# Kernel optimization log

Measured on AMD Instinct MI355X. Metric: run time of the kernel, lower is better.

Reference implementation:

```python
import jax, jax.numpy as jnp
import numpy as np

# Dimensions (Gemma-2B-like, uniform q-head rank)
B, S, HID = 2, 2048, 2048
H, HKV, D = 16, 8, 128
RQ, RK, RV = 64, 64, 64
G = H // HKV  # heads per kv group
SCALE = D ** -0.5
NEG_INF = -1e9


def setup_inputs() -> dict:
    key = jax.random.key(0)
    ks = jax.random.split(key, 9)
    hidden_states = jax.random.normal(ks[0], (B, S, HID), dtype=jnp.float32)
    W_A_q = jax.random.normal(ks[1], (H * RQ, HID), dtype=jnp.float32) * 0.02
    W_A_k = jax.random.normal(ks[2], (HKV * RK, HID), dtype=jnp.float32) * 0.02
    W_A_v = jax.random.normal(ks[3], (HKV * RV, HID), dtype=jnp.float32) * 0.02
    B_q = jax.random.normal(ks[4], (H, RQ, D), dtype=jnp.float32)
    B_k = jax.random.normal(ks[5], (HKV, RK, D), dtype=jnp.float32)
    B_v = jax.random.normal(ks[6], (HKV, RV, D), dtype=jnp.float32)
    W_o = jax.random.normal(ks[7], (HID, H * D), dtype=jnp.float32) * 0.02
    # RoPE tables (cos/sin form of gemma's complex freqs_cis)
    inv_freq = 1.0 / (10000.0 ** (jnp.arange(0, D, 2, dtype=jnp.float32) / D))
    freqs = jnp.arange(S, dtype=jnp.float32)[:, None] * inv_freq[None, :]  # [S, D/2]
    freqs_cos = jnp.cos(freqs)
    freqs_sin = jnp.sin(freqs)
    # Causal additive mask [1, 1, S, S]
    causal = jnp.tril(jnp.ones((S, S), dtype=bool))
    mask = jnp.where(causal, 0.0, NEG_INF).astype(jnp.float32)[None, None]
    kv_write_indices = jnp.arange(S, dtype=jnp.int32)
    return {
        'hidden_states': hidden_states, 'W_A_q': W_A_q, 'W_A_k': W_A_k,
        'W_A_v': W_A_v, 'B_q': B_q, 'B_k': B_k, 'B_v': B_v, 'W_o': W_o,
        'freqs_cos': freqs_cos, 'freqs_sin': freqs_sin, 'mask': mask,
        'kv_write_indices': kv_write_indices,
    }


def _rope(x, cos, sin):
    # x: [b, s, h, d]; gemma pairs first half with second half of head_dim
    x1, x2 = jnp.split(x, 2, axis=-1)
    c = cos[None, :, None, :]
    s = sin[None, :, None, :]
    return jnp.concatenate([x1 * c - x2 * s, x1 * s + x2 * c], axis=-1)


def reference(hidden_states, W_A_q, W_A_k, W_A_v, B_q, B_k, B_v, W_o,
              freqs_cos, freqs_sin, mask, kv_write_indices):
    b, s, _ = hidden_states.shape
    # Low-rank A factors
    A_q = jnp.einsum('bsd,rd->bsr', hidden_states, W_A_q).reshape(b, s, H, RQ)
    A_k = jnp.einsum('bsd,rd->bsr', hidden_states, W_A_k).reshape(b, s, HKV, RK)
    A_v = jnp.einsum('bsd,rd->bsr', hidden_states, W_A_v).reshape(b, s, HKV, RV)
    # Factorized KV cache: scatter A factors at write indices (prefill)
    cache_kA = jnp.zeros((b, s, HKV, RK), hidden_states.dtype).at[:, kv_write_indices].set(A_k)
    cache_vA = jnp.zeros((b, s, HKV, RV), hidden_states.dtype).at[:, kv_write_indices].set(A_v)
    # GQA expansion of cached A factors
    gidx = jnp.repeat(jnp.arange(HKV), G)  # [H]
    A_k_rep = cache_kA[:, :, gidx]  # [b, kv, H, RK]
    A_v_rep = cache_vA[:, :, gidx]
    # Reconstruct Q/K/V from constant B factors (per-head loop vectorized:
    # all q ranks equal, so einsum over heads is the same math)
    q = jnp.einsum('bshr,hrd->bshd', A_q, B_q) / RQ
    k = jnp.einsum('bkhr,hrd->bkhd', A_k_rep, B_k[gidx]) / RK
    v = jnp.einsum('bkhr,hrd->bkhd', A_v_rep, B_v[gidx]) / RV
    # RoPE post-reconstruction
    q = _rope(q, freqs_cos, freqs_sin)
    k = _rope(k, freqs_cos, freqs_sin)
    # Attention
    scores = jnp.einsum('bqhd,bkhd->bhqk', q, k) * SCALE + mask
    probs = jax.nn.softmax(scores, axis=-1)
    out = jnp.einsum('bhqk,bkhd->bqhd', probs, v).reshape(b, s, H * D)
    return jnp.einsum('bse,he->bsh', out, W_o)
```

## Files before the change

kernel.cpp:

```cpp
#include <hip/hip_runtime.h>
#include <hip/hip_bf16.h>

typedef __attribute__((ext_vector_type(8))) short bf16x8;
typedef __attribute__((ext_vector_type(4))) float f32x4;

#define MFMA_16x16x32(a,b,c) __builtin_amdgcn_mfma_f32_16x16x32_bf16((a),(b),(c),0,0,0)

__device__ __forceinline__ unsigned short f2b(float f){
  unsigned int u = __builtin_bit_cast(unsigned int, f);
  u = u + 0x7FFFu + ((u >> 16) & 1u);
  return (unsigned short)(u >> 16);
}
__device__ __forceinline__ float b2f(unsigned short h){
  unsigned int u = ((unsigned int)h) << 16;
  return __builtin_bit_cast(float, u);
}

__device__ __forceinline__ void gload_lds16(const unsigned short* g, unsigned short* l){
  __builtin_amdgcn_global_load_lds(
      (const __attribute__((address_space(1))) void*)g,
      (__attribute__((address_space(3))) void*)l, 16, 0, 0);
}


__global__ void cvt_f32_bf16(const float* __restrict__ src, unsigned short* __restrict__ dst, int n4){
  int i = blockIdx.x * blockDim.x + threadIdx.x;
  int stride = gridDim.x * blockDim.x;
  for (; i < n4; i += stride){
    float4 v = reinterpret_cast<const float4*>(src)[i];
    ushort4 o;
    o.x = f2b(v.x); o.y = f2b(v.y); o.z = f2b(v.z); o.w = f2b(v.w);
    reinterpret_cast<ushort4*>(dst)[i] = o;
  }
}

__global__ void cvt_factor_t(const float* __restrict__ src, unsigned short* __restrict__ dst, int n){
  int i = blockIdx.x * blockDim.x + threadIdx.x;
  if (i >= n) return;
  int d = i & 127, r = (i >> 7) & 63, h = i >> 13;
  dst[(h << 13) + (d << 6) + r] = f2b(src[i]);
}

__global__ void rope_inplace(unsigned short* __restrict__ buf,
                             const float* __restrict__ fc,
                             const float* __restrict__ fs, int total){
  int i = blockIdx.x * blockDim.x + threadIdx.x;
  if (i >= total) return;
  int d4 = (i & 15) << 2;
  int s  = (i >> 4) & 2047;
  size_t base = ((size_t)(i >> 4)) * 128;
  ushort4 x1 = *reinterpret_cast<ushort4*>(buf + base + d4);
  ushort4 x2 = *reinterpret_cast<ushort4*>(buf + base + 64 + d4);
  float4 c  = *reinterpret_cast<const float4*>(fc + (size_t)s*64 + d4);
  float4 sn = *reinterpret_cast<const float4*>(fs + (size_t)s*64 + d4);
  ushort4 o1, o2; float a, b;
  a = b2f(x1.x); b = b2f(x2.x); o1.x = f2b(a*c.x - b*sn.x); o2.x = f2b(a*sn.x + b*c.x);
  a = b2f(x1.y); b = b2f(x2.y); o1.y = f2b(a*c.y - b*sn.y); o2.y = f2b(a*sn.y + b*c.y);
  a = b2f(x1.z); b = b2f(x2.z); o1.z = f2b(a*c.z - b*sn.z); o2.z = f2b(a*sn.z + b*c.z);
  a = b2f(x1.w); b = b2f(x2.w); o1.w = f2b(a*c.w - b*sn.w); o2.w = f2b(a*sn.w + b*c.w);
  *reinterpret_cast<ushort4*>(buf + base + d4)      = o1;
  *reinterpret_cast<ushort4*>(buf + base + 64 + d4) = o2;
}


template<int OUT_F32>
__global__ __launch_bounds__(256) void gemm_bt(
    const unsigned short* __restrict__ A, const unsigned short* __restrict__ B,
    void* __restrict__ Cv, int N, int K, float scale)
{
  __shared__ unsigned short As[2][128*64];
  __shared__ unsigned short Bs[2][128*64];
  const int tid = threadIdx.x;
  const int mb = blockIdx.x, nb = blockIdx.y;
  const int w = tid >> 6, lane = tid & 63;
  const int wr = w >> 1, wc = w & 1;
  const int l16 = lane & 15, lg = lane >> 4;

  f32x4 acc[4][4] = {};

  const unsigned short* Ap = A + (size_t)(mb*128)*K;
  const unsigned short* Bp = B + (size_t)(nb*128)*K;

  const int sRo = 32*w + (lane >> 3);
  const int sCo = ((lane & 7) ^ (lane >> 3)) << 3;
  const int ldsW = 2048*w;

  auto stage = [&](int kt, int buf){
    const unsigned short* Ak = Ap + (size_t)kt*64 + sCo;
    const unsigned short* Bk = Bp + (size_t)kt*64 + sCo;
    #pragma unroll
    for (int i = 0; i < 4; i++)
      gload_lds16(Ak + (size_t)(sRo + 8*i)*K, &As[buf][ldsW + 512*i]);
    #pragma unroll
    for (int i = 0; i < 4; i++)
      gload_lds16(Bk + (size_t)(sRo + 8*i)*K, &Bs[buf][ldsW + 512*i]);
  };

  const int nkt = K >> 6;
  stage(0, 0);
  __syncthreads();

  int cur = 0;
  for (int kt = 0; kt < nkt; kt++){
    if (kt + 1 < nkt) stage(kt + 1, cur ^ 1);
    #pragma unroll
    for (int t = 0; t < 2; t++){
      bf16x8 af[4], bf[4];
      #pragma unroll
      for (int i = 0; i < 4; i++){
        int rowA = wr*64 + i*16 + l16;
        int col  = t*32 + lg*8;
        af[i] = *reinterpret_cast<const bf16x8*>(&As[cur][(rowA*64 + col) ^ ((rowA & 7) << 3)]);
        int rowB = wc*64 + i*16 + l16;
        bf[i] = *reinterpret_cast<const bf16x8*>(&Bs[cur][(rowB*64 + col) ^ ((rowB & 7) << 3)]);
      }
      #pragma unroll
      for (int i = 0; i < 4; i++)
        #pragma unroll
        for (int j = 0; j < 4; j++)
          acc[i][j] = MFMA_16x16x32(af[i], bf[j], acc[i][j]);
    }
    __syncthreads();
    cur ^= 1;
  }

  #pragma unroll
  for (int i = 0; i < 4; i++){
    #pragma unroll
    for (int j = 0; j < 4; j++){
      int row = mb*128 + wr*64 + i*16 + lg*4;
      int col = nb*128 + wc*64 + j*16 + l16;
      #pragma unroll
      for (int r = 0; r < 4; r++){
        float v = acc[i][j][r] * scale;
        if (OUT_F32) reinterpret_cast<float*>(Cv)[(size_t)(row + r)*N + col] = v;
        else reinterpret_cast<unsigned short*>(Cv)[(size_t)(row + r)*N + col] = f2b(v);
      }
    }
  }
}


__global__ __launch_bounds__(256) void factor_gemm(
    const unsigned short* __restrict__ A,
    const unsigned short* __restrict__ Bt,
    unsigned short* __restrict__ Out, int coloff, int Hn, float scale)
{
  __shared__ unsigned short As[128*64];
  __shared__ unsigned short Bs[128*64];
  const int tid = threadIdx.x;
  const int mb = blockIdx.x;
  const int h  = blockIdx.y;
  const int w = tid >> 6, lane = tid & 63;
  const int wr = w >> 1, wc = w & 1;
  const int l16 = lane & 15, lg = lane >> 4;

  const int srow = tid >> 3;
  const int scol = (tid & 7) << 3;

  const unsigned short* Ap = A + (size_t)(mb*128)*2048 + coloff + h*64;
  const unsigned short* Bp = Bt + (size_t)h*(128*64);

  #pragma unroll
  for (int c = 0; c < 4; c++){
    int r = srow + 32*c;
    int idx = (r*64 + scol) ^ ((r & 7) << 3);
    *reinterpret_cast<bf16x8*>(&As[idx]) = *reinterpret_cast<const bf16x8*>(Ap + (size_t)r*2048 + scol);
    *reinterpret_cast<bf16x8*>(&Bs[idx]) = *reinterpret_cast<const bf16x8*>(Bp + r*64 + scol);
  }
  __syncthreads();

  f32x4 acc[4][4] = {};
  #pragma unroll
  for (int t = 0; t < 2; t++){
    bf16x8 af[4], bf[4];
    #pragma unroll
    for (int i = 0; i < 4; i++){
      int rowA = wr*64 + i*16 + l16;
      int col  = t*32 + lg*8;
      af[i] = *reinterpret_cast<const bf16x8*>(&As[(rowA*64 + col) ^ ((rowA & 7) << 3)]);
      int rowB = wc*64 + i*16 + l16;
      bf[i] = *reinterpret_cast<const bf16x8*>(&Bs[(rowB*64 + col) ^ ((rowB & 7) << 3)]);
    }
    #pragma unroll
    for (int i = 0; i < 4; i++)
      #pragma unroll
      for (int j = 0; j < 4; j++)
        acc[i][j] = MFMA_16x16x32(af[i], bf[j], acc[i][j]);
  }

  #pragma unroll
  for (int i = 0; i < 4; i++){
    #pragma unroll
    for (int j = 0; j < 4; j++){
      int row0 = mb*128 + wr*64 + i*16 + lg*4;
      int d    = wc*64 + j*16 + l16;
      #pragma unroll
      for (int r = 0; r < 4; r++){
        int row = row0 + r;
        int b = row >> 11, s = row & 2047;
        Out[((size_t)(b*Hn + h)*2048 + s)*128 + d] = f2b(acc[i][j][r] * scale);
      }
    }
  }
}


__device__ __forceinline__ int vt_idx(int d, int kv){
  return d*64 + ((((kv >> 3) + d + (d >> 3)) & 7) << 3) + (kv & 7);
}

__global__ __launch_bounds__(256) void flash_attn(
    const unsigned short* __restrict__ Q,
    const unsigned short* __restrict__ Kb,
    const unsigned short* __restrict__ Vb,
    unsigned short* __restrict__ O)
{
  __shared__ unsigned short Ks[64*128];
  __shared__ unsigned short Vrow[64*128];
  __shared__ unsigned short Vt[128*64];
  __shared__ unsigned short Pl[4][16*64];

  const int tid = threadIdx.x;
  const int w = tid >> 6, lane = tid & 63;
  const int l16 = lane & 15, lg = lane >> 4;
  const int h = blockIdx.y, b = blockIdx.z;
  const int hkv = h >> 1;

  const size_t hbase  = ((size_t)(b*16 + h))*2048*128;
  const size_t kvbase = ((size_t)(b*8 + hkv))*2048*128;

  const int sR = w*16 + (lane >> 4);
  const int sC = (lane & 15) * 8;

  auto stage = [&](int kb){
    #pragma unroll
    for (int i = 0; i < 4; i++){
      int R = sR + i*4;
      const unsigned short* gk = Kb + kvbase + (size_t)(kb*64 + R)*128 + (sC ^ ((R & 7) << 3));
      gload_lds16(gk, &Ks[(w*16 + i*4)*128]);
      const unsigned short* gv = Vb + kvbase + (size_t)(kb*64 + R)*128 + sC;
      gload_lds16(gv, &Vrow[(w*16 + i*4)*128]);
    }
  };

  stage(0);
  __syncthreads();

  const int tkv0 = (tid >> 4) * 4;
  const int td0  = (tid & 15) * 8;

  const int qtiles[2] = { (int)blockIdx.x, 31 - (int)blockIdx.x };

  for (int ph = 0; ph < 2; ph++){
    const int qe = qtiles[ph];
    const size_t qbase = hbase + (size_t)(qe*64 + w*16)*128;
    const int qrow0 = qe*64 + w*16 + lg*4;

    bf16x8 aq[4];
    #pragma unroll
    for (int t = 0; t < 4; t++)
      aq[t] = *reinterpret_cast<const bf16x8*>(&Q[qbase + (size_t)l16*128 + t*32 + lg*8]);

    f32x4 oac[8] = {};
    float mrow[4], lrow[4];
    #pragma unroll
    for (int r = 0; r < 4; r++){ mrow[r] = -1e30f; lrow[r] = 0.f; }

    for (int kb = 0; kb <= qe; kb++){
      bf16x8 vr0 = *reinterpret_cast<const bf16x8*>(&Vrow[(tkv0 + 0)*128 + td0]);
      bf16x8 vr1 = *reinterpret_cast<const bf16x8*>(&Vrow[(tkv0 + 1)*128 + td0]);
      bf16x8 vr2 = *reinterpret_cast<const bf16x8*>(&Vrow[(tkv0 + 2)*128 + td0]);
      bf16x8 vr3 = *reinterpret_cast<const bf16x8*>(&Vrow[(tkv0 + 3)*128 + td0]);

      f32x4 sac[4] = {};
      #pragma unroll
      for (int nt = 0; nt < 4; nt++){
        #pragma unroll
        for (int t = 0; t < 4; t++){
          int rowK = nt*16 + l16;
          int col  = t*32 + lg*8;
          bf16x8 bk = *reinterpret_cast<const bf16x8*>(&Ks[(rowK*128 + col) ^ ((rowK & 7) << 3)]);
          sac[nt] = MFMA_16x16x32(aq[t], bk, sac[nt]);
        }
      }

      #pragma unroll
      for (int j = 0; j < 8; j++){
        unsigned int lo = (unsigned int)(unsigned short)vr0[j] | ((unsigned int)(unsigned short)vr1[j] << 16);
        unsigned int hi = (unsigned int)(unsigned short)vr2[j] | ((unsigned int)(unsigned short)vr3[j] << 16);
        uint2 u; u.x = lo; u.y = hi;
        *reinterpret_cast<uint2*>(&Vt[vt_idx(td0 + j, tkv0)]) = u;
      }

      if (kb == qe){
        #pragma unroll
        for (int nt = 0; nt < 4; nt++){
          int kcol = kb*64 + nt*16 + l16;
          #pragma unroll
          for (int r = 0; r < 4; r++)
            if (kcol > qrow0 + r) sac[nt][r] = -1e30f;
        }
      }
      float corr[4];
      #pragma unroll
      for (int r = 0; r < 4; r++){
        float v = fmaxf(fmaxf(sac[0][r], sac[1][r]), fmaxf(sac[2][r], sac[3][r]));
        v = fmaxf(v, __shfl_xor(v, 1));
        v = fmaxf(v, __shfl_xor(v, 2));
        v = fmaxf(v, __shfl_xor(v, 4));
        v = fmaxf(v, __shfl_xor(v, 8));
        float mn = fmaxf(mrow[r], v);
        corr[r] = __expf(mrow[r] - mn);
        mrow[r] = mn;
      }
      float rs[4] = {0.f, 0.f, 0.f, 0.f};
      #pragma unroll
      for (int nt = 0; nt < 4; nt++){
        #pragma unroll
        for (int r = 0; r < 4; r++){
          float p = __expf(sac[nt][r] - mrow[r]);
          sac[nt][r] = p;
          rs[r] += p;
        }
      }
      #pragma unroll
      for (int r = 0; r < 4; r++){
        float v = rs[r];
        v += __shfl_xor(v, 1); v += __shfl_xor(v, 2); v += __shfl_xor(v, 4); v += __shfl_xor(v, 8);
        lrow[r] = lrow[r]*corr[r] + v;
      }
      #pragma unroll
      for (int dn = 0; dn < 8; dn++)
        #pragma unroll
        for (int r = 0; r < 4; r++) oac[dn][r] *= corr[r];

      #pragma unroll
      for (int nt = 0; nt < 4; nt++){
        #pragma unroll
        for (int r = 0; r < 4; r++){
          int row = lg*4 + r, col = nt*16 + l16;
          Pl[w][(row*64 + col) ^ ((row & 7) << 3)] = f2b(sac[nt][r]);
        }
      }

      __syncthreads();
      if (kb < qe) stage(kb + 1);
      else if (ph == 0) stage(0);

      #pragma unroll
      for (int t = 0; t < 2; t++){
        int colp = t*32 + lg*8;
        bf16x8 ap = *reinterpret_cast<const bf16x8*>(&Pl[w][(l16*64 + colp) ^ ((l16 & 7) << 3)]);
        #pragma unroll
        for (int dn = 0; dn < 8; dn++){
          int rowV = dn*16 + l16;
          bf16x8 bv = *reinterpret_cast<const bf16x8*>(&Vt[vt_idx(rowV, colp)]);
          oac[dn] = MFMA_16x16x32(ap, bv, oac[dn]);
        }
      }
      __syncthreads();
    }

    #pragma unroll
    for (int dn = 0; dn < 8; dn++){
      #pragma unroll
      for (int r = 0; r < 4; r++){
        int row = qe*64 + w*16 + lg*4 + r;
        O[((size_t)(b*2048 + row))*2048 + h*128 + dn*16 + l16] = f2b(oac[dn][r] / lrow[r]);
      }
    }
  }
}


extern "C" void kernel_launch(void* const* d_in, const int* in_sizes, int n_in,
                              void* d_out, int out_size, void* d_ws, size_t ws_size,
                              hipStream_t stream)
{
  if (n_in < 10) return;
  const float* hidden = (const float*)d_in[0];
  const float* WAq = (const float*)d_in[1];
  const float* WAk = (const float*)d_in[2];
  const float* WAv = (const float*)d_in[3];
  const float* Bq  = (const float*)d_in[4];
  const float* Bk  = (const float*)d_in[5];
  const float* Bv  = (const float*)d_in[6];
  const float* Wo  = (const float*)d_in[7];
  const float* fcos = (const float*)d_in[8];
  const float* fsin = (const float*)d_in[9];
  float* out = (float*)d_out;

  char* p = (char*)d_ws;
  auto take = [&](size_t bytes){ char* q = p; p += (bytes + 255) & ~(size_t)255; return q; };
  unsigned short* Xb   = (unsigned short*)take((size_t)4096*2048*2);
  unsigned short* Wqkv = (unsigned short*)take((size_t)2048*2048*2);
  unsigned short* Wob  = (unsigned short*)take((size_t)2048*2048*2);
  unsigned short* Aqkv = (unsigned short*)take((size_t)4096*2048*2);
  unsigned short* Bqt  = (unsigned short*)take((size_t)16*128*64*2);
  unsigned short* Bkt  = (unsigned short*)take((size_t)8*128*64*2);
  unsigned short* Bvt  = (unsigned short*)take((size_t)8*128*64*2);
  unsigned short* qbuf = (unsigned short*)take((size_t)2*16*2048*128*2);
  unsigned short* kbuf = (unsigned short*)take((size_t)2*8*2048*128*2);
  unsigned short* vbuf = (unsigned short*)take((size_t)2*8*2048*128*2);
  unsigned short* aout = (unsigned short*)take((size_t)4096*2048*2);
  if ((size_t)(p - (char*)d_ws) > ws_size) return;

  auto cvt = [&](const float* s, unsigned short* d, size_t n){
    int n4 = (int)(n >> 2);
    int blocks = (n4 + 255) / 256; if (blocks > 4096) blocks = 4096;
    cvt_f32_bf16<<<blocks, 256, 0, stream>>>(s, d, n4);
  };
  cvt(hidden, Xb, (size_t)4096*2048);
  cvt(WAq, Wqkv,                       (size_t)1024*2048);
  cvt(WAk, Wqkv + (size_t)1024*2048,   (size_t)512*2048);
  cvt(WAv, Wqkv + (size_t)1536*2048,   (size_t)512*2048);
  cvt(Wo,  Wob, (size_t)2048*2048);
  cvt_factor_t<<<(16*64*128)/256, 256, 0, stream>>>(Bq, Bqt, 16*64*128);
  cvt_factor_t<<<(8*64*128)/256, 256, 0, stream>>>(Bk, Bkt, 8*64*128);
  cvt_factor_t<<<(8*64*128)/256, 256, 0, stream>>>(Bv, Bvt, 8*64*128);

  gemm_bt<0><<<dim3(32,16), 256, 0, stream>>>(Xb, Wqkv, (void*)Aqkv, 2048, 2048, 1.0f);

  const float SCALE = 0.08838834764831845f;
  factor_gemm<<<dim3(32,16), 256, 0, stream>>>(Aqkv, Bqt, qbuf, 0,    16, SCALE/64.0f);
  factor_gemm<<<dim3(32,8),  256, 0, stream>>>(Aqkv, Bkt, kbuf, 1024, 8,  1.0f/64.0f);
  factor_gemm<<<dim3(32,8),  256, 0, stream>>>(Aqkv, Bvt, vbuf, 1536, 8,  1.0f/64.0f);

  rope_inplace<<<(32*2048*16)/256, 256, 0, stream>>>(qbuf, fcos, fsin, 32*2048*16);
  rope_inplace<<<(16*2048*16)/256, 256, 0, stream>>>(kbuf, fcos, fsin, 16*2048*16);

  flash_attn<<<dim3(16,16,2), 256, 0, stream>>>(qbuf, kbuf, vbuf, aout);

  gemm_bt<1><<<dim3(32,16), 256, 0, stream>>>(aout, Wob, (void*)out, 2048, 2048, 1.0f);
}
```

Before: 384.7 us.

## Fuse conversions into batched kernels and fold RoPE into factor GEMM epilogue

Merges the five fp32->bf16 conversion launches into one grid-stride kernel and the three factor transposes into one launch. The three factor GEMMs and two RoPE passes become a single launch. Each wave now owns a 32-row strip across all 128 head dims, so the first- and second-half outputs of a row sit in one thread and RoPE can be applied in registers before the store. This removes about ten launches and a read-modify-write pass over q and k. In exchange it adds branchy index selection in the convert kernel and per-element cos/sin global loads in the epilogue.

```diff
diff --git a/kernel.cpp b/kernel.cpp
--- a/kernel.cpp
+++ b/kernel.cpp
@@ -23,43 +23,43 @@
 }
 
 
-__global__ void cvt_f32_bf16(const float* __restrict__ src, unsigned short* __restrict__ dst, int n4){
+__global__ void cvt_all(const float* __restrict__ hid, const float* __restrict__ wq,
+                        const float* __restrict__ wk, const float* __restrict__ wv,
+                        const float* __restrict__ wo,
+                        unsigned short* __restrict__ Xb, unsigned short* __restrict__ Wqkv,
+                        unsigned short* __restrict__ Wob){
+  const int N0 = 2097152, N1 = 524288, N2 = 262144, N3 = 262144, N4 = 1048576;
+  const int E1 = N0 + N1, E2 = E1 + N2, E3 = E2 + N3, E4 = E3 + N4;
   int i = blockIdx.x * blockDim.x + threadIdx.x;
-  int stride = gridDim.x * blockDim.x;
-  for (; i < n4; i += stride){
-    float4 v = reinterpret_cast<const float4*>(src)[i];
+  const int stride = gridDim.x * blockDim.x;
+  for (; i < E4; i += stride){
+    const float* s; unsigned short* d; int off;
+    if (i < N0)      { s = hid; d = Xb;   off = i; }
+    else if (i < E1) { s = wq;  d = Wqkv; off = i - N0; }
+    else if (i < E2) { s = wk;  d = Wqkv; off = i - E1 + 524288;  s = wk;  }
+    else if (i < E3) { s = wv;  d = Wqkv; off = i - E2 + 786432; }
+    else             { s = wo;  d = Wob;  off = i - E3; }
+    int src_off = (i < N0) ? i : (i < E1) ? (i - N0) : (i < E2) ? (i - E1) : (i < E3) ? (i - E2) : (i - E3);
+    float4 v = reinterpret_cast<const float4*>(s)[src_off];
     ushort4 o;
     o.x = f2b(v.x); o.y = f2b(v.y); o.z = f2b(v.z); o.w = f2b(v.w);
-    reinterpret_cast<ushort4*>(dst)[i] = o;
-  }
-}
-
-__global__ void cvt_factor_t(const float* __restrict__ src, unsigned short* __restrict__ dst, int n){
+    reinterpret_cast<ushort4*>(d)[off] = o;
+  }
+}
+
+__global__ void cvt_factors(const float* __restrict__ Bq, const float* __restrict__ Bk,
+                            const float* __restrict__ Bv,
+                            unsigned short* __restrict__ Bqt, unsigned short* __restrict__ Bkt,
+                            unsigned short* __restrict__ Bvt){
   int i = blockIdx.x * blockDim.x + threadIdx.x;
-  if (i >= n) return;
-  int d = i & 127, r = (i >> 7) & 63, h = i >> 13;
-  dst[(h << 13) + (d << 6) + r] = f2b(src[i]);
-}
-
-__global__ void rope_inplace(unsigned short* __restrict__ buf,
-                             const float* __restrict__ fc,
-                             const float* __restrict__ fs, int total){
-  int i = blockIdx.x * blockDim.x + threadIdx.x;
-  if (i >= total) return;
-  int d4 = (i & 15) << 2;
-  int s  = (i >> 4) & 2047;
-  size_t base = ((size_t)(i >> 4)) * 128;
-  ushort4 x1 = *reinterpret_cast<ushort4*>(buf + base + d4);
-  ushort4 x2 = *reinterpret_cast<ushort4*>(buf + base + 64 + d4);
-  float4 c  = *reinterpret_cast<const float4*>(fc + (size_t)s*64 + d4);
-  float4 sn = *reinterpret_cast<const float4*>(fs + (size_t)s*64 + d4);
-  ushort4 o1, o2; float a, b;
-  a = b2f(x1.x); b = b2f(x2.x); o1.x = f2b(a*c.x - b*sn.x); o2.x = f2b(a*sn.x + b*c.x);
-  a = b2f(x1.y); b = b2f(x2.y); o1.y = f2b(a*c.y - b*sn.y); o2.y = f2b(a*sn.y + b*c.y);
-  a = b2f(x1.z); b = b2f(x2.z); o1.z = f2b(a*c.z - b*sn.z); o2.z = f2b(a*sn.z + b*c.z);
-  a = b2f(x1.w); b = b2f(x2.w); o1.w = f2b(a*c.w - b*sn.w); o2.w = f2b(a*sn.w + b*c.w);
-  *reinterpret_cast<ushort4*>(buf + base + d4)      = o1;
-  *reinterpret_cast<ushort4*>(buf + base + 64 + d4) = o2;
+  if (i >= 32*8192) return;
+  int H = i >> 13, e = i & 8191;
+  int d = e & 127, r = (e >> 7) & 63;
+  const float* src; unsigned short* dst; int h;
+  if (H < 16)      { src = Bq; dst = Bqt; h = H; }
+  else if (H < 24) { src = Bk; dst = Bkt; h = H - 16; }
+  else             { src = Bv; dst = Bvt; h = H - 24; }
+  dst[(h << 13) + (d << 6) + r] = f2b(src[(size_t)(h << 13) + e]);
 }
 
 
@@ -141,65 +141,83 @@
 }
 
 
-__global__ __launch_bounds__(256) void factor_gemm(
+__global__ __launch_bounds__(256) void factor_rope(
     const unsigned short* __restrict__ A,
-    const unsigned short* __restrict__ Bt,
-    unsigned short* __restrict__ Out, int coloff, int Hn, float scale)
+    const unsigned short* __restrict__ Bqt, const unsigned short* __restrict__ Bkt,
+    const unsigned short* __restrict__ Bvt,
+    unsigned short* __restrict__ qb, unsigned short* __restrict__ kb2,
+    unsigned short* __restrict__ vb,
+    const float* __restrict__ fc, const float* __restrict__ fs)
 {
   __shared__ unsigned short As[128*64];
   __shared__ unsigned short Bs[128*64];
-  const int tid = threadIdx.x;
-  const int mb = blockIdx.x;
-  const int h  = blockIdx.y;
+  const int tid = threadIdx.x, mb = blockIdx.x, H = blockIdx.y;
   const int w = tid >> 6, lane = tid & 63;
-  const int wr = w >> 1, wc = w & 1;
   const int l16 = lane & 15, lg = lane >> 4;
+  const float SCALE = 0.08838834764831845f;
+
+  int h, coloff, Hn; const unsigned short* Bt; unsigned short* Out; float scale; bool rope;
+  if (H < 16)      { h = H;      coloff = h*64;        Hn = 16; Bt = Bqt + (size_t)h*8192; Out = qb;  scale = SCALE/64.f; rope = true; }
+  else if (H < 24) { h = H - 16; coloff = 1024 + h*64; Hn = 8;  Bt = Bkt + (size_t)h*8192; Out = kb2; scale = 1.f/64.f;   rope = true; }
+  else             { h = H - 24; coloff = 1536 + h*64; Hn = 8;  Bt = Bvt + (size_t)h*8192; Out = vb;  scale = 1.f/64.f;   rope = false; }
 
   const int srow = tid >> 3;
   const int scol = (tid & 7) << 3;
-
-  const unsigned short* Ap = A + (size_t)(mb*128)*2048 + coloff + h*64;
-  const unsigned short* Bp = Bt + (size_t)h*(128*64);
+  const unsigned short* Ap = A + (size_t)(mb*128)*2048 + coloff;
 
   #pragma unroll
   for (int c = 0; c < 4; c++){
     int r = srow + 32*c;
     int idx = (r*64 + scol) ^ ((r & 7) << 3);
     *reinterpret_cast<bf16x8*>(&As[idx]) = *reinterpret_cast<const bf16x8*>(Ap + (size_t)r*2048 + scol);
-    *reinterpret_cast<bf16x8*>(&Bs[idx]) = *reinterpret_cast<const bf16x8*>(Bp + r*64 + scol);
+    *reinterpret_cast<bf16x8*>(&Bs[idx]) = *reinterpret_cast<const bf16x8*>(Bt + r*64 + scol);
   }
   __syncthreads();
 
-  f32x4 acc[4][4] = {};
+  f32x4 acc[2][8] = {};
   #pragma unroll
   for (int t = 0; t < 2; t++){
-    bf16x8 af[4], bf[4];
-    #pragma unroll
-    for (int i = 0; i < 4; i++){
-      int rowA = wr*64 + i*16 + l16;
+    bf16x8 af[2], bf[8];
+    #pragma unroll
+    for (int i = 0; i < 2; i++){
+      int rowA = w*32 + i*16 + l16;
       int col  = t*32 + lg*8;
       af[i] = *reinterpret_cast<const bf16x8*>(&As[(rowA*64 + col) ^ ((rowA & 7) << 3)]);
-      int rowB = wc*64 + i*16 + l16;
-      bf[i] = *reinterpret_cast<const bf16x8*>(&Bs[(rowB*64 + col) ^ ((rowB & 7) << 3)]);
-    }
-    #pragma unroll
-    for (int i = 0; i < 4; i++)
-      #pragma unroll
-      for (int j = 0; j < 4; j++)
+    }
+    #pragma unroll
+    for (int j = 0; j < 8; j++){
+      int rowB = j*16 + l16;
+      int col  = t*32 + lg*8;
+      bf[j] = *reinterpret_cast<const bf16x8*>(&Bs[(rowB*64 + col) ^ ((rowB & 7) << 3)]);
+    }
+    #pragma unroll
+    for (int i = 0; i < 2; i++)
+      #pragma unroll
+      for (int j = 0; j < 8; j++)
         acc[i][j] = MFMA_16x16x32(af[i], bf[j], acc[i][j]);
   }
 
   #pragma unroll
-  for (int i = 0; i < 4; i++){
+  for (int i = 0; i < 2; i++){
     #pragma unroll
     for (int j = 0; j < 4; j++){
-      int row0 = mb*128 + wr*64 + i*16 + lg*4;
-      int d    = wc*64 + j*16 + l16;
+      int d = j*16 + l16;
       #pragma unroll
       for (int r = 0; r < 4; r++){
-        int row = row0 + r;
-        int b = row >> 11, s = row & 2047;
-        Out[((size_t)(b*Hn + h)*2048 + s)*128 + d] = f2b(acc[i][j][r] * scale);
+        int row = mb*128 + w*32 + i*16 + lg*4 + r;
+        int s = row & 2047, bb = row >> 11;
+        float lo = acc[i][j][r] * scale;
+        float hi = acc[i][j+4][r] * scale;
+        float o1, o2;
+        if (rope){
+          float cc = fc[(size_t)s*64 + d];
+          float ss = fs[(size_t)s*64 + d];
+          o1 = lo*cc - hi*ss;
+          o2 = lo*ss + hi*cc;
+        } else { o1 = lo; o2 = hi; }
+        size_t base = ((size_t)(bb*Hn + h)*2048 + s)*128;
+        Out[base + d]      = f2b(o1);
+        Out[base + 64 + d] = f2b(o2);
       }
     }
   }
@@ -406,29 +424,12 @@
   unsigned short* aout = (unsigned short*)take((size_t)4096*2048*2);
   if ((size_t)(p - (char*)d_ws) > ws_size) return;
 
-  auto cvt = [&](const float* s, unsigned short* d, size_t n){
-    int n4 = (int)(n >> 2);
-    int blocks = (n4 + 255) / 256; if (blocks > 4096) blocks = 4096;
-    cvt_f32_bf16<<<blocks, 256, 0, stream>>>(s, d, n4);
-  };
-  cvt(hidden, Xb, (size_t)4096*2048);
-  cvt(WAq, Wqkv,                       (size_t)1024*2048);
-  cvt(WAk, Wqkv + (size_t)1024*2048,   (size_t)512*2048);
-  cvt(WAv, Wqkv + (size_t)1536*2048,   (size_t)512*2048);
-  cvt(Wo,  Wob, (size_t)2048*2048);
-  cvt_factor_t<<<(16*64*128)/256, 256, 0, stream>>>(Bq, Bqt, 16*64*128);
-  cvt_factor_t<<<(8*64*128)/256, 256, 0, stream>>>(Bk, Bkt, 8*64*128);
-  cvt_factor_t<<<(8*64*128)/256, 256, 0, stream>>>(Bv, Bvt, 8*64*128);
+  cvt_all<<<4096, 256, 0, stream>>>(hidden, WAq, WAk, WAv, Wo, Xb, Wqkv, Wob);
+  cvt_factors<<<1024, 256, 0, stream>>>(Bq, Bk, Bv, Bqt, Bkt, Bvt);
 
   gemm_bt<0><<<dim3(32,16), 256, 0, stream>>>(Xb, Wqkv, (void*)Aqkv, 2048, 2048, 1.0f);
 
-  const float SCALE = 0.08838834764831845f;
-  factor_gemm<<<dim3(32,16), 256, 0, stream>>>(Aqkv, Bqt, qbuf, 0,    16, SCALE/64.0f);
-  factor_gemm<<<dim3(32,8),  256, 0, stream>>>(Aqkv, Bkt, kbuf, 1024, 8,  1.0f/64.0f);
-  factor_gemm<<<dim3(32,8),  256, 0, stream>>>(Aqkv, Bvt, vbuf, 1536, 8,  1.0f/64.0f);
-
-  rope_inplace<<<(32*2048*16)/256, 256, 0, stream>>>(qbuf, fcos, fsin, 32*2048*16);
-  rope_inplace<<<(16*2048*16)/256, 256, 0, stream>>>(kbuf, fcos, fsin, 16*2048*16);
+  factor_rope<<<dim3(32,32), 256, 0, stream>>>(Aqkv, Bqt, Bkt, Bvt, qbuf, kbuf, vbuf, fcos, fsin);
 
   flash_attn<<<dim3(16,16,2), 256, 0, stream>>>(qbuf, kbuf, vbuf, aout);
 
```

New measurement: 357.9 us. 7.0% less time.
